# Performance work log

Measured on AMD Instinct MI355X. Metric: run time of the kernel, lower is better.

The kernel has to match this reference:

```python
import jax, jax.numpy as jnp
import numpy as np

N = 10000      # atoms
E = 100000     # edges
C = 64         # hidden channels
S = 16         # spherical harmonic components (l_max=3)
NB = 8         # Bessel basis size
HID = 64       # radial MLP hidden
NE = 10        # chemical elements
G = 64         # graphs in batch
L = 2          # interaction layers
HEADS = 1
RC = 5.0       # radial cutoff
AVG_NEI = 16.0


def _sph_l3(u):
    # real spherical harmonics up to l=3, component normalization, on unit vectors u [E,3]
    x, y, z = u[..., 0], u[..., 1], u[..., 2]
    s3 = 3.0 ** 0.5; s5 = 5.0 ** 0.5; s15 = 15.0 ** 0.5
    c1 = (35.0 / 8.0) ** 0.5; c2 = 105.0 ** 0.5; c3 = (21.0 / 8.0) ** 0.5
    c4 = (7.0 / 4.0) ** 0.5; c5 = (105.0 / 4.0) ** 0.5
    comps = [jnp.ones_like(x),
             s3 * x, s3 * y, s3 * z,
             s15 * x * y, s15 * y * z, (s5 / 2) * (3 * z * z - 1), s15 * x * z, (s15 / 2) * (x * x - y * y),
             c1 * y * (3 * x * x - y * y), c2 * x * y * z, c3 * y * (5 * z * z - 1), c4 * z * (5 * z * z - 3),
             c3 * x * (5 * z * z - 1), c5 * z * (x * x - y * y), c1 * x * (x * x - 3 * y * y)]
    return jnp.stack(comps, axis=-1)  # [E, 16]


def _radial(r):
    # Bessel radial basis * polynomial cutoff (p=6); r [E,1] -> [E, NB]
    n = jnp.arange(1, NB + 1, dtype=r.dtype)
    bessel = (2.0 / RC) ** 0.5 * jnp.sin(n * jnp.pi * r / RC) / r
    t = r / RC
    p = 6.0
    fcut = 1.0 - (p + 1) * (p + 2) / 2 * t ** p + p * (p + 2) * t ** (p + 1) - p * (p + 1) / 2 * t ** (p + 2)
    fcut = jnp.where(r < RC, fcut, 0.0)
    return bessel * fcut


def setup_inputs() -> dict:
    key = jax.random.key(0)
    ks = jax.random.split(key, 20)
    positions = jax.random.uniform(ks[0], (N, 3), dtype=jnp.float32) * 6.0
    species = jax.random.randint(ks[1], (N,), 0, NE)
    node_attrs = jax.nn.one_hot(species, NE, dtype=jnp.float32)
    sender = jax.random.randint(ks[2], (E,), 0, N)
    offs = jax.random.randint(ks[3], (E,), 1, N)
    receiver = (sender + offs) % N  # no self loops
    edge_index = jnp.stack([sender, receiver]).astype(jnp.int32)
    batch = jnp.sort(jax.random.randint(ks[4], (N,), 0, G)).astype(jnp.int32)
    head = jnp.zeros((G,), jnp.int32)
    shifts = jnp.zeros((E, 3), jnp.float32)
    ptr = jnp.arange(G + 1, dtype=jnp.int32)
    w = 0.1
    return {
        'positions': positions, 'node_attrs': node_attrs, 'shifts': shifts,
        'atomic_energies': jax.random.normal(ks[5], (HEADS, NE), jnp.float32),
        'W_emb': w * jax.random.normal(ks[6], (NE, C), jnp.float32),
        'W_up': w * jax.random.normal(ks[7], (L, C, C), jnp.float32),
        'mlp_w1': w * jax.random.normal(ks[8], (L, NB, HID), jnp.float32),
        'mlp_w2': w * jax.random.normal(ks[9], (L, HID, HID), jnp.float32),
        'mlp_w3': w * jax.random.normal(ks[10], (L, HID, C * S), jnp.float32),
        'W_mix': w * jax.random.normal(ks[11], (L, C, C), jnp.float32),
        'W_skip': w * jax.random.normal(ks[12], (L, C, NE, C), jnp.float32),
        'Wc': w * jax.random.normal(ks[13], (L, NE, 3, C), jnp.float32),
        'W_out': w * jax.random.normal(ks[14], (L, C, C), jnp.float32),
        'W_ro': w * jax.random.normal(ks[15], (L, C, HEADS), jnp.float32),
        'edge_index': edge_index, 'batch': batch, 'head': head, 'ptr': ptr,
    }


def reference(positions, node_attrs, shifts, atomic_energies, W_emb, W_up, mlp_w1,
              mlp_w2, mlp_w3, W_mix, W_skip, Wc, W_out, W_ro,
              edge_index, batch, head, ptr):
    n_nodes = positions.shape[0]
    n_graphs = ptr.shape[0] - 1
    sender, receiver = edge_index[0], edge_index[1]
    na = jnp.arange(n_nodes)
    node_heads = head[batch]                                   # [N]
    # isolated-atom reference energies
    node_e0 = (node_attrs @ atomic_energies.T)[na, node_heads]  # [N]
    e0 = jax.ops.segment_sum(node_e0, batch, num_segments=n_graphs)
    node_feats = node_attrs @ W_emb                            # [N, C]
    # edge geometry: gather positions by edge index
    vectors = positions[receiver] - positions[sender] + shifts  # [E, 3]
    lengths = jnp.sqrt(jnp.sum(vectors ** 2, axis=-1, keepdims=True))  # [E, 1]
    edge_attrs = _sph_l3(vectors / lengths)                    # [E, S]
    edge_feats = _radial(lengths)                              # [E, NB]
    energies = [e0, jnp.zeros_like(e0)]  # e0, pair_energy (no pair_repulsion)
    for l in range(W_up.shape[0]):
        # radial MLP -> per-edge tensor-product weights
        h = jax.nn.silu(edge_feats @ mlp_w1[l])
        h = jax.nn.silu(h @ mlp_w2[l])
        tp_w = (h @ mlp_w3[l]).reshape(-1, C, S)               # [E, C, S]
        up = node_feats @ W_up[l]                              # [N, C]
        # gather-compute-scatter message passing
        msg = up[sender][:, :, None] * edge_attrs[:, None, :] * tp_w  # [E, C, S]
        A = jax.ops.segment_sum(msg, receiver, num_segments=n_nodes) / AVG_NEI
        A = jnp.einsum('ncs,cd->nds', A, W_mix[l])             # [N, C, S]
        # element-conditioned skip connection
        sc = jnp.einsum('nc,ced,ne->nd', node_feats, W_skip[l], node_attrs)
        # symmetric-contraction product basis (correlation up to 3), element-conditioned
        w = jnp.einsum('ne,ekc->nkc', node_attrs, Wc[l])       # [N, 3, C]
        p1 = A[:, :, 0]
        p2 = jnp.einsum('ncs,ncs->nc', A, A)
        p3 = p2 * p1
        node_feats = (w[:, 0] * p1 + w[:, 1] * p2 + w[:, 2] * p3) @ W_out[l] + sc
        node_en = (node_feats @ W_ro[l])[na, node_heads]       # [N]
        energies.append(jax.ops.segment_sum(node_en, batch, num_segments=n_graphs))
    contributions = jnp.stack(energies, axis=-1)               # [G, L+2]
    return jnp.sum(contributions, axis=-1)                     # [G]
```

## Files before the change

### kernel.cpp

```cpp
#include <hip/hip_runtime.h>

typedef unsigned short u16;
typedef unsigned int u32;
typedef __attribute__((ext_vector_type(8))) short short8;
typedef __attribute__((ext_vector_type(4))) float f32x4;

#define N_NODES 10000
#define N_EDGES 100000
#define C_CH 64
#define S_SPH 16
#define NB_R 8
#define HID_D 64
#define NE_EL 10
#define G_GR 64
#define L_LAY 2
#define N_HEADS 1
#define RCUT 5.0f
#define INV_AVG (1.0f/16.0f)

__device__ __forceinline__ u16 f2bf(float f) {
  u32 u = __float_as_uint(f);
  u32 r = (u + 0x7FFFu + ((u >> 16) & 1u)) >> 16;
  return (u16)r;
}

__global__ void k_init0(float* __restrict__ out, int* __restrict__ deg) {
  int i = blockIdx.x * 256 + threadIdx.x;
  if (i < G_GR) out[i] = 0.0f;
  if (i < N_NODES) deg[i] = 0;
}

__global__ void k_node_init(const float* __restrict__ attrs, const float* __restrict__ ae,
                            const int* __restrict__ batch, const int* __restrict__ head,
                            int* __restrict__ species, float* __restrict__ out) {
  int n = blockIdx.x * 256 + threadIdx.x;
  if (n >= N_NODES) return;
  int sp = 0;
#pragma unroll
  for (int e = 0; e < NE_EL; ++e)
    if (attrs[n * NE_EL + e] > 0.5f) sp = e;
  species[n] = sp;
  int b = batch[n];
  int h = head[b];
  atomicAdd(&out[b], ae[h * NE_EL + sp]);
}

__global__ void k_embed(const int* __restrict__ species, const float* __restrict__ Wemb,
                        float* __restrict__ feats) {
  int idx = blockIdx.x * 256 + threadIdx.x;
  if (idx >= N_NODES * C_CH) return;
  feats[idx] = Wemb[species[idx >> 6] * C_CH + (idx & 63)];
}

__global__ void k_hist(const int* __restrict__ ei, int* __restrict__ deg) {
  int e = blockIdx.x * 256 + threadIdx.x;
  if (e >= N_EDGES) return;
  atomicAdd(&deg[ei[N_EDGES + e]], 1);
}

__global__ void __launch_bounds__(1024) k_scan(const int* __restrict__ deg,
                                               int* __restrict__ rowptr,
                                               int* __restrict__ woff) {
  __shared__ int wsum[16];
  __shared__ int carry_s;
  int tid = threadIdx.x;
  int lane = tid & 63, w = tid >> 6;
  if (tid == 0) carry_s = 0;
  __syncthreads();
  for (int base = 0; base < N_NODES; base += 1024) {
    int i = base + tid;
    int v = (i < N_NODES) ? deg[i] : 0;
    int orig = v;
#pragma unroll
    for (int off = 1; off < 64; off <<= 1) {
      int n = __shfl_up(v, off, 64);
      if (lane >= off) v += n;
    }
    if (lane == 63) wsum[w] = v;
    __syncthreads();
    if (w == 0 && lane < 16) {
      int x = wsum[lane];
#pragma unroll
      for (int off = 1; off < 16; off <<= 1) {
        int n = __shfl_up(x, off, 16);
        if (lane >= off) x += n;
      }
      wsum[lane] = x;
    }
    __syncthreads();
    int waveoff = (w > 0) ? wsum[w - 1] : 0;
    int carry = carry_s;
    int excl = carry + waveoff + v - orig;
    if (i < N_NODES) {
      rowptr[i] = excl;
      woff[i] = excl;
    }
    int tot = wsum[15];
    __syncthreads();
    if (tid == 0) carry_s = carry + tot;
    __syncthreads();
  }
  if (tid == 0) rowptr[N_NODES] = carry_s;
}

__global__ void k_permute(const int* __restrict__ ei, int* __restrict__ woff,
                          int* __restrict__ rank, int* __restrict__ sndp) {
  int e = blockIdx.x * 256 + threadIdx.x;
  if (e >= N_EDGES) return;
  int rdst = ei[N_EDGES + e];
  int pos = atomicAdd(&woff[rdst], 1);
  rank[e] = pos;
  sndp[pos] = ei[e];
}

__global__ void k_geom(const float* __restrict__ pos, const float* __restrict__ shifts,
                       const int* __restrict__ ei, const int* __restrict__ rank,
                       float* __restrict__ Yp, float* __restrict__ radp) {
  int e = blockIdx.x * 256 + threadIdx.x;
  if (e >= N_EDGES) return;
  int s = ei[e], r = ei[N_EDGES + e];
  float dx = pos[r * 3 + 0] - pos[s * 3 + 0] + shifts[e * 3 + 0];
  float dy = pos[r * 3 + 1] - pos[s * 3 + 1] + shifts[e * 3 + 1];
  float dz = pos[r * 3 + 2] - pos[s * 3 + 2] + shifts[e * 3 + 2];
  float rr = sqrtf(dx * dx + dy * dy + dz * dz);
  rr = fmaxf(rr, 1e-12f);
  float inv = 1.0f / rr;
  float x = dx * inv, y = dy * inv, z = dz * inv;
  float xx = x * x, yy = y * y, zz = z * z;
  const float s3 = 1.73205080757f, s5 = 2.2360679775f, s15 = 3.87298334621f;
  const float c1 = 2.09165006634f, c2 = 10.2469507659f, c3 = 1.62018517461f;
  const float c4 = 1.32287565553f, c5 = 5.12347538298f;
  int rk = rank[e];
  float4* Yo = (float4*)(Yp + (size_t)rk * 16);
  Yo[0] = make_float4(1.0f, s3 * x, s3 * y, s3 * z);
  Yo[1] = make_float4(s15 * x * y, s15 * y * z, 0.5f * s5 * (3.0f * zz - 1.0f), s15 * x * z);
  Yo[2] = make_float4(0.5f * s15 * (xx - yy), c1 * y * (3.0f * xx - yy), c2 * x * y * z,
                      c3 * y * (5.0f * zz - 1.0f));
  Yo[3] = make_float4(c4 * z * (5.0f * zz - 3.0f), c3 * x * (5.0f * zz - 1.0f),
                      c5 * z * (xx - yy), c1 * x * (xx - 3.0f * yy));
  float t = rr * (1.0f / RCUT);
  float t2 = t * t;
  float t6 = t2 * t2 * t2;
  float fcut = 1.0f - 28.0f * t6 + 48.0f * t6 * t - 21.0f * t6 * t2;
  if (rr >= RCUT) fcut = 0.0f;
  float pref = 0.63245553203f * inv * fcut;
  float arg = 3.14159265359f * rr * (1.0f / RCUT);
  float sa, ca;
  __sincosf(arg, &sa, &ca);
  float twoc = 2.0f * ca;
  float sprev = 0.0f, scur = sa;
  float rv[8];
#pragma unroll
  for (int n = 0; n < 8; ++n) {
    rv[n] = pref * scur;
    float snext = twoc * scur - sprev;
    sprev = scur;
    scur = snext;
  }
  float4* Ro = (float4*)(radp + (size_t)rk * 8);
  Ro[0] = make_float4(rv[0], rv[1], rv[2], rv[3]);
  Ro[1] = make_float4(rv[4], rv[5], rv[6], rv[7]);
}

__global__ void k_prep(const float* __restrict__ w3, const float* __restrict__ w2,
                       const float* __restrict__ wmix, const float* __restrict__ wskip,
                       u16* __restrict__ w3t, u16* __restrict__ w2t, u16* __restrict__ wmixf,
                       float* __restrict__ wskt) {
  int idx = blockIdx.x * 256 + threadIdx.x;
  if (idx < L_LAY * 65536) {
    int l = idx >> 16;
    int r = idx & 65535;
    int k = r & 63;
    int c = (r >> 6) & 63;
    int s = r >> 12;
    w3t[idx] = f2bf(w3[(l * 64 + k) * 1024 + c * 16 + s]);
  } else if (idx < L_LAY * 65536 + L_LAY * 4096) {
    int i = idx - L_LAY * 65536;
    int l = i >> 12;
    int r = i & 4095;
    int t = r >> 6;
    int j = r & 63;
    w2t[l * 4096 + t * 64 + j] = f2bf(w2[(l * 64 + j) * 64 + t]);
  } else if (idx < L_LAY * 65536 + 2 * L_LAY * 4096) {
    int i = idx - L_LAY * 65536 - L_LAY * 4096;
    int l = i >> 12;
    int r = i & 4095;
    int j = r & 7;
    int col = (r >> 3) & 15;
    int kg = (r >> 7) & 3;
    int hf = (r >> 9) & 1;
    int dc = (r >> 10) & 3;
    int c = hf * 32 + kg * 8 + j;
    int d = dc * 16 + col;
    wmixf[l * 4096 + r] = f2bf(wmix[(l * 64 + c) * 64 + d]);
  } else if (idx < L_LAY * 65536 + 2 * L_LAY * 4096 + L_LAY * 40960) {
    int i = idx - (L_LAY * 65536 + 2 * L_LAY * 4096);
    int l = (i >= 40960) ? 1 : 0;
    int r = i - l * 40960;
    int e = r >> 12;
    int rem = r & 4095;
    int c = rem >> 6;
    int d = rem & 63;
    wskt[(size_t)l * 40960 + e * 4096 + c * 64 + d] =
        wskip[(size_t)l * 40960 + c * 640 + e * 64 + d];
  }
}

__global__ void __launch_bounds__(64) k_edge_mlp(const float* __restrict__ radp,
                                                 const float* __restrict__ w1,
                                                 const u16* __restrict__ w2T,
                                                 u16* __restrict__ h2) {
  __shared__ float w1s[NB_R * HID_D];
  __shared__ __align__(16) u16 h1b[16 * 64];
  int lane = threadIdx.x;
  for (int i = lane; i < NB_R * HID_D; i += 64) w1s[i] = w1[i];
  int er = lane & 15, jg = lane >> 4;
  int eb = blockIdx.x * 16;
  int e = eb + er;
  float4 ra = *(const float4*)(radp + (size_t)e * 8);
  float4 rb = *(const float4*)(radp + (size_t)e * 8 + 4);
  float rv[8] = {ra.x, ra.y, ra.z, ra.w, rb.x, rb.y, rb.z, rb.w};
  u32* hb = (u32*)h1b;
#pragma unroll
  for (int jj = 0; jj < 16; jj += 2) {
    float p0 = 0.f, p1 = 0.f;
#pragma unroll
    for (int k = 0; k < 8; ++k) {
      p0 += rv[k] * w1s[k * 64 + jg * 16 + jj];
      p1 += rv[k] * w1s[k * 64 + jg * 16 + jj + 1];
    }
    p0 = p0 / (1.f + __expf(-p0));
    p1 = p1 / (1.f + __expf(-p1));
    u32 packed = (u32)f2bf(p0) | ((u32)f2bf(p1) << 16);
    int d = jg * 8 + (jj >> 1);
    hb[er * 32 + (d ^ ((er & 7) << 2))] = packed;
  }
  int row = er, kg = jg, col = er;
  const u32* hbr = (const u32*)h1b;
  short8 a0 = *(const short8*)&hbr[row * 32 + ((kg * 4) ^ ((row & 7) << 2))];
  short8 a1 = *(const short8*)&hbr[row * 32 + ((16 + kg * 4) ^ ((row & 7) << 2))];
#pragma unroll
  for (int ch = 0; ch < 4; ++ch) {
    const u16* wp = w2T + (ch * 16 + col) * 64 + kg * 8;
    short8 b0 = *(const short8*)wp;
    short8 b1 = *(const short8*)(wp + 32);
    f32x4 acc = {0.f, 0.f, 0.f, 0.f};
    acc = __builtin_amdgcn_mfma_f32_16x16x32_bf16(a0, b0, acc, 0, 0, 0);
    acc = __builtin_amdgcn_mfma_f32_16x16x32_bf16(a1, b1, acc, 0, 0, 0);
#pragma unroll
    for (int rr = 0; rr < 4; ++rr) {
      float v = acc[rr];
      v = v / (1.f + __expf(-v));
      h2[(size_t)(eb + kg * 4 + rr) * 64 + ch * 16 + col] = f2bf(v);
    }
  }
}

__global__ void __launch_bounds__(256) k_up(const float* __restrict__ feats,
                                            const float* __restrict__ Wup,
                                            float* __restrict__ up) {
  __shared__ float ws[C_CH * C_CH];
  __shared__ float fs[4][C_CH];
  int tid = threadIdx.x;
  for (int i = tid; i < C_CH * C_CH; i += 256) ws[i] = Wup[i];
  __syncthreads();
  int slot = tid >> 6, t = tid & 63;
  for (int nb = blockIdx.x * 4; nb < N_NODES; nb += gridDim.x * 4) {
    int n = nb + slot;
    fs[slot][t] = feats[n * C_CH + t];
    float acc = 0.0f;
#pragma unroll
    for (int j = 0; j < C_CH; ++j) acc += fs[slot][j] * ws[j * C_CH + t];
    up[n * C_CH + t] = acc * INV_AVG;
  }
}

__global__ void __launch_bounds__(256) k_upe(const float* __restrict__ up,
                                             const int* __restrict__ sndp,
                                             float* __restrict__ upe) {
  int tid = threadIdx.x;
  int slot = tid >> 6, t = tid & 63;
  for (int pb = blockIdx.x * 4; pb < N_EDGES; pb += gridDim.x * 4) {
    int pos = pb + slot;
    upe[(size_t)pos * 64 + t] = up[(size_t)sndp[pos] * 64 + t];
  }
}

__global__ void __launch_bounds__(256) k_gather_fused(
    const u16* __restrict__ h2, const u16* __restrict__ W3T, const float* __restrict__ upe,
    const float* __restrict__ Yp, const int* __restrict__ rowptr,
    const u16* __restrict__ WmixF, const float* __restrict__ featsOld,
    float* __restrict__ featsNew, const float* __restrict__ WskT,
    const float* __restrict__ Wc, const float* __restrict__ WoutG,
    const float* __restrict__ Wro, const int* __restrict__ species,
    const int* __restrict__ batch, const int* __restrict__ headArr,
    float* __restrict__ out) {
  __shared__ __align__(16) u16 h2s[128 * 64];
  __shared__ __align__(16) float Yts[16][128];
  __shared__ __align__(16) u16 Asub[4][16][72];
  __shared__ float qs[4][64];
  __shared__ float fsub[4][64];
  __shared__ int rps[5];
  int tid = threadIdx.x;
  int wv = tid >> 6, lane = tid & 63;
  int row = lane & 15, kg = lane >> 4;
  int col = row;
  int cg = wv;
  int cgc = cg * 16 + col;
  int nb = blockIdx.x * 4;
  if (tid < 5) rps[tid] = rowptr[nb + tid];
  fsub[wv][lane] = featsOld[(size_t)(nb + wv) * 64 + lane];
  __syncthreads();
  int rp0 = rps[0], rp1 = rps[1], rp2 = rps[2], rp3 = rps[3], rp4 = rps[4];
  int d0 = rp1 - rp0, d1 = rp2 - rp1, d2 = rp3 - rp2, d3 = rp4 - rp3;
  int rmax = max(max((d0 + 3) >> 2, (d1 + 3) >> 2), max((d2 + 3) >> 2, (d3 + 3) >> 2));
  rmax = max(rmax, 1);
  int baseR = kg == 0 ? rp0 : kg == 1 ? rp1 : kg == 2 ? rp2 : rp3;
  int degR = kg == 0 ? d0 : kg == 1 ? d1 : kg == 2 ? d2 : d3;

  float Areg[2][8];
#pragma unroll
  for (int hf = 0; hf < 2; ++hf)
#pragma unroll
    for (int ss = 0; ss < 8; ++ss) Areg[hf][ss] = 0.f;

  const u32* h2sr = (const u32*)h2s;

#pragma unroll 1
  for (int r0 = 0; r0 < rmax; r0 += 8) {
    int CH = min(8, rmax - r0);
    int shift = (CH > 4) ? 5 : 4;
    int nrows = 4 << shift;
    __syncthreads();
    for (int j = tid; j < nrows * 8; j += 256) {
      int rrow = j >> 3, part = j & 7;
      int node = rrow >> shift;
      int sl = r0 * 4 + (rrow & ((1 << shift) - 1));
      int e = min(rps[node] + sl, N_EDGES - 1);
      short8 v = *(const short8*)(h2 + (size_t)e * 64 + part * 8);
      int dsw = (part * 4) ^ (((rrow ^ (rrow >> 3)) & 7) << 2);
      *(short8*)((u32*)h2s + rrow * 32 + dsw) = v;
    }
    for (int j = tid; j < nrows * 4; j += 256) {
      int rrow = j >> 2, part = j & 3;
      int node = rrow >> shift;
      int sl = r0 * 4 + (rrow & ((1 << shift) - 1));
      int e = min(rps[node] + sl, N_EDGES - 1);
      float4 y = *(const float4*)(Yp + (size_t)e * 16 + part * 4);
      Yts[part * 4 + 0][rrow] = y.x;
      Yts[part * 4 + 1][rrow] = y.y;
      Yts[part * 4 + 2][rrow] = y.z;
      Yts[part * 4 + 3][rrow] = y.w;
    }
    __syncthreads();
#pragma unroll 1
    for (int hf = 0; hf < 2; ++hf) {
      short8 B0[8], B1[8];
#pragma unroll
      for (int ss = 0; ss < 8; ++ss) {
        int s = hf * 8 + ss;
        const u16* wp = W3T + (((s * 64 + cg * 16 + col) << 6) + kg * 8);
        B0[ss] = *(const short8*)wp;
        B1[ss] = *(const short8*)(wp + 32);
      }
#pragma unroll 1
      for (int rl = 0; rl < CH; ++rl) {
        int srow = ((row >> 2) << shift) + rl * 4 + (row & 3);
        int swz = (((srow ^ (srow >> 3)) & 7) << 2);
        short8 a0 = *(const short8*)(h2sr + srow * 32 + ((kg * 4) ^ swz));
        short8 a1 = *(const short8*)(h2sr + srow * 32 + ((16 + kg * 4) ^ swz));
        int slq = (r0 + rl) * 4;
        float upv[4];
#pragma unroll
        for (int q = 0; q < 4; ++q) {
          int pos = min(baseR + slq + q, N_EDGES - 1);
          float u = upe[(size_t)pos * 64 + cgc];
          upv[q] = (slq + q < degR) ? u : 0.f;
        }
        int ybase = (kg << shift) + rl * 4;
#pragma unroll
        for (int ss = 0; ss < 8; ++ss) {
          f32x4 acc = {0.f, 0.f, 0.f, 0.f};
          acc = __builtin_amdgcn_mfma_f32_16x16x32_bf16(a0, B0[ss], acc, 0, 0, 0);
          acc = __builtin_amdgcn_mfma_f32_16x16x32_bf16(a1, B1[ss], acc, 0, 0, 0);
          float4 yv = *(const float4*)&Yts[hf * 8 + ss][ybase];
          Areg[hf][ss] += acc[0] * yv.x * upv[0] + acc[1] * yv.y * upv[1] +
                          acc[2] * yv.z * upv[2] + acc[3] * yv.w * upv[3];
        }
      }
    }
  }
#pragma unroll
  for (int hf = 0; hf < 2; ++hf)
#pragma unroll
    for (int ss = 0; ss < 8; ++ss) Asub[kg][hf * 8 + ss][cg * 16 + col] = f2bf(Areg[hf][ss]);
  __syncthreads();

  int sp = species[nb + wv];
  short8 a0m = *(const short8*)&Asub[wv][row][kg * 8];
  short8 a1m = *(const short8*)&Asub[wv][row][32 + kg * 8];
#pragma unroll
  for (int dc = 0; dc < 4; ++dc) {
    short8 wf0 = *(const short8*)(WmixF + (size_t)(dc * 1024 + 0 * 512 + kg * 128 + row * 8));
    short8 wf1 = *(const short8*)(WmixF + (size_t)(dc * 1024 + 1 * 512 + kg * 128 + row * 8));
    f32x4 acc = {0.f, 0.f, 0.f, 0.f};
    acc = __builtin_amdgcn_mfma_f32_16x16x32_bf16(a0m, wf0, acc, 0, 0, 0);
    acc = __builtin_amdgcn_mfma_f32_16x16x32_bf16(a1m, wf1, acc, 0, 0, 0);
    float psq = acc[0] * acc[0] + acc[1] * acc[1] + acc[2] * acc[2] + acc[3] * acc[3];
    psq += __shfl_xor(psq, 16, 64);
    psq += __shfl_xor(psq, 32, 64);
    float p1 = __shfl(acc[0], lane & 15, 64);
    float p3 = psq * p1;
    int d = dc * 16 + row;
    float qv = Wc[(sp * 3 + 0) * 64 + d] * p1 + Wc[(sp * 3 + 1) * 64 + d] * psq +
               Wc[(sp * 3 + 2) * 64 + d] * p3;
    if (kg == 0) qs[wv][d] = qv;
  }

  int t = lane;
  const float* wsk = WskT + (size_t)sp * 4096;
  float sc = 0.f;
#pragma unroll 8
  for (int c = 0; c < 64; ++c) sc += fsub[wv][c] * wsk[c * 64 + t];
  float v = sc;
#pragma unroll 8
  for (int d = 0; d < 64; ++d) v += qs[wv][d] * WoutG[d * 64 + t];
  featsNew[(size_t)(nb + wv) * 64 + t] = v;
  int b = batch[nb + wv];
  float en = v * Wro[t * N_HEADS + headArr[b]];
#pragma unroll
  for (int off = 32; off; off >>= 1) en += __shfl_down(en, off, 64);
  if (lane == 0) atomicAdd(&out[b], en);
}

extern "C" void kernel_launch(void* const* d_in, const int* in_sizes, int n_in,
                              void* d_out, int out_size, void* d_ws, size_t ws_size,
                              hipStream_t stream) {
  const float* pos = (const float*)d_in[0];
  const float* attrs = (const float*)d_in[1];
  const float* shifts = (const float*)d_in[2];
  const float* ae = (const float*)d_in[3];
  const float* Wemb = (const float*)d_in[4];
  const float* Wup = (const float*)d_in[5];
  const float* w1 = (const float*)d_in[6];
  const float* w2 = (const float*)d_in[7];
  const float* w3 = (const float*)d_in[8];
  const float* Wmix = (const float*)d_in[9];
  const float* Wskip = (const float*)d_in[10];
  const float* Wc = (const float*)d_in[11];
  const float* Wout = (const float*)d_in[12];
  const float* Wro = (const float*)d_in[13];
  const int* ei = (const int*)d_in[14];
  const int* batch = (const int*)d_in[15];
  const int* head = (const int*)d_in[16];
  float* out = (float*)d_out;

  char* p = (char*)d_ws;
  float* Yp = (float*)p;     p += (size_t)N_EDGES * 16 * 4;
  float* radp = (float*)p;   p += (size_t)N_EDGES * 8 * 4;
  float* up = (float*)p;     p += (size_t)N_NODES * 64 * 4;
  float* upe = (float*)p;    p += (size_t)N_EDGES * 64 * 4;
  float* fA = (float*)p;     p += (size_t)N_NODES * 64 * 4;
  float* fB = (float*)p;     p += (size_t)N_NODES * 64 * 4;
  u16* h2 = (u16*)p;         p += (size_t)N_EDGES * 64 * 2;
  u16* W3T = (u16*)p;        p += (size_t)L_LAY * 65536 * 2;
  u16* w2T = (u16*)p;        p += (size_t)L_LAY * 4096 * 2;
  u16* WmixF = (u16*)p;      p += (size_t)L_LAY * 4096 * 2;
  float* WskT = (float*)p;   p += (size_t)L_LAY * 40960 * 4;
  int* species = (int*)p;    p += (size_t)N_NODES * 4;
  int* deg = (int*)p;        p += (size_t)N_NODES * 4;
  int* rowptr = (int*)p;     p += (size_t)(N_NODES + 4) * 4;
  int* woff = (int*)p;       p += (size_t)N_NODES * 4;
  int* rank = (int*)p;       p += (size_t)N_EDGES * 4;
  int* sndp = (int*)p;       p += (size_t)N_EDGES * 4;
  if ((size_t)(p - (char*)d_ws) > ws_size) return;

  k_init0<<<(N_NODES + 255) / 256, 256, 0, stream>>>(out, deg);
  k_node_init<<<(N_NODES + 255) / 256, 256, 0, stream>>>(attrs, ae, batch, head, species, out);
  k_embed<<<(N_NODES * C_CH + 255) / 256, 256, 0, stream>>>(species, Wemb, fA);
  k_hist<<<(N_EDGES + 255) / 256, 256, 0, stream>>>(ei, deg);
  k_scan<<<1, 1024, 0, stream>>>(deg, rowptr, woff);
  k_permute<<<(N_EDGES + 255) / 256, 256, 0, stream>>>(ei, woff, rank, sndp);
  k_geom<<<(N_EDGES + 255) / 256, 256, 0, stream>>>(pos, shifts, ei, rank, Yp, radp);
  int prepTot = L_LAY * 65536 + 2 * L_LAY * 4096 + L_LAY * 40960;
  k_prep<<<(prepTot + 255) / 256, 256, 0, stream>>>(w3, w2, Wmix, Wskip, W3T, w2T, WmixF, WskT);

  const float* fOld = fA;
  float* fNew = fB;
  for (int l = 0; l < L_LAY; ++l) {
    k_edge_mlp<<<N_EDGES / 16, 64, 0, stream>>>(radp, w1 + l * NB_R * HID_D, w2T + l * 4096, h2);
    k_up<<<512, 256, 0, stream>>>(fOld, Wup + l * C_CH * C_CH, up);
    k_upe<<<2048, 256, 0, stream>>>(up, sndp, upe);
    k_gather_fused<<<N_NODES / 4, 256, 0, stream>>>(
        h2, W3T + l * 65536, upe, Yp, rowptr, WmixF + l * 4096, fOld, fNew,
        WskT + (size_t)l * 40960, Wc + l * NE_EL * 3 * C_CH, Wout + l * C_CH * C_CH,
        Wro + l * C_CH * N_HEADS, species, batch, head, out);
    const float* tmp = fNew;
    fNew = (float*)fOld;
    fOld = tmp;
  }
}
```

Baseline: 452.0 us.

## Sort nodes by degree for balanced gather blocks and prefetch up values

Adds a counting sort of nodes by descending in-degree (bins, scan, scatter) so each gather block of four nodes processes nodes with similar degree, reducing padding wasted on the max-degree node. The gather kernel now uses fixed 4-row chunks with smaller shared tiles and prefetches the per-edge up values into registers before the staging barrier. This costs three extra small kernel launches and makes per-node reads and writes scattered instead of contiguous.

```diff
diff --git a/kernel.cpp b/kernel.cpp
--- a/kernel.cpp
+++ b/kernel.cpp
@@ -24,9 +24,10 @@
   return (u16)r;
 }
 
-__global__ void k_init0(float* __restrict__ out, int* __restrict__ deg) {
+__global__ void k_init0(float* __restrict__ out, int* __restrict__ deg, int* __restrict__ bins) {
   int i = blockIdx.x * 256 + threadIdx.x;
   if (i < G_GR) out[i] = 0.0f;
+  if (i < 64) bins[i] = 0;
   if (i < N_NODES) deg[i] = 0;
 }
 
@@ -101,6 +102,35 @@
     __syncthreads();
   }
   if (tid == 0) rowptr[N_NODES] = carry_s;
+}
+
+__global__ void k_degbin(const int* __restrict__ deg, int* __restrict__ bins) {
+  int n = blockIdx.x * 256 + threadIdx.x;
+  if (n >= N_NODES) return;
+  int d = min(deg[n], 63);
+  atomicAdd(&bins[63 - d], 1);
+}
+
+__global__ void __launch_bounds__(64) k_degscan(const int* __restrict__ bins,
+                                                int* __restrict__ binoff) {
+  int lane = threadIdx.x;
+  int v = bins[lane];
+  int orig = v;
+#pragma unroll
+  for (int off = 1; off < 64; off <<= 1) {
+    int t = __shfl_up(v, off, 64);
+    if (lane >= off) v += t;
+  }
+  binoff[lane] = v - orig;
+}
+
+__global__ void k_degscatter(const int* __restrict__ deg, int* __restrict__ binoff,
+                             int* __restrict__ nodeOrder) {
+  int n = blockIdx.x * 256 + threadIdx.x;
+  if (n >= N_NODES) return;
+  int d = min(deg[n], 63);
+  int pos = atomicAdd(&binoff[63 - d], 1);
+  nodeOrder[pos] = n;
 }
 
 __global__ void k_permute(const int* __restrict__ ei, int* __restrict__ woff,
@@ -289,18 +319,18 @@
 __global__ void __launch_bounds__(256) k_gather_fused(
     const u16* __restrict__ h2, const u16* __restrict__ W3T, const float* __restrict__ upe,
     const float* __restrict__ Yp, const int* __restrict__ rowptr,
-    const u16* __restrict__ WmixF, const float* __restrict__ featsOld,
-    float* __restrict__ featsNew, const float* __restrict__ WskT,
-    const float* __restrict__ Wc, const float* __restrict__ WoutG,
-    const float* __restrict__ Wro, const int* __restrict__ species,
-    const int* __restrict__ batch, const int* __restrict__ headArr,
-    float* __restrict__ out) {
-  __shared__ __align__(16) u16 h2s[128 * 64];
-  __shared__ __align__(16) float Yts[16][128];
+    const int* __restrict__ nodeOrder, const u16* __restrict__ WmixF,
+    const float* __restrict__ featsOld, float* __restrict__ featsNew,
+    const float* __restrict__ WskT, const float* __restrict__ Wc,
+    const float* __restrict__ WoutG, const float* __restrict__ Wro,
+    const int* __restrict__ species, const int* __restrict__ batch,
+    const int* __restrict__ headArr, float* __restrict__ out) {
+  __shared__ __align__(16) u16 h2s[64 * 64];
+  __shared__ __align__(16) float Yts[16][68];
   __shared__ __align__(16) u16 Asub[4][16][72];
   __shared__ float qs[4][64];
   __shared__ float fsub[4][64];
-  __shared__ int rps[5];
+  __shared__ int rpsA[4], rpsB[4];
   int tid = threadIdx.x;
   int wv = tid >> 6, lane = tid & 63;
   int row = lane & 15, kg = lane >> 4;
@@ -308,15 +338,19 @@
   int cg = wv;
   int cgc = cg * 16 + col;
   int nb = blockIdx.x * 4;
-  if (tid < 5) rps[tid] = rowptr[nb + tid];
-  fsub[wv][lane] = featsOld[(size_t)(nb + wv) * 64 + lane];
+  int nodeW = nodeOrder[nb + wv];
+  if (tid < 4) {
+    int n = nodeOrder[nb + tid];
+    rpsA[tid] = rowptr[n];
+    rpsB[tid] = rowptr[n + 1];
+  }
+  fsub[wv][lane] = featsOld[(size_t)nodeW * 64 + lane];
   __syncthreads();
-  int rp0 = rps[0], rp1 = rps[1], rp2 = rps[2], rp3 = rps[3], rp4 = rps[4];
-  int d0 = rp1 - rp0, d1 = rp2 - rp1, d2 = rp3 - rp2, d3 = rp4 - rp3;
-  int rmax = max(max((d0 + 3) >> 2, (d1 + 3) >> 2), max((d2 + 3) >> 2, (d3 + 3) >> 2));
-  rmax = max(rmax, 1);
-  int baseR = kg == 0 ? rp0 : kg == 1 ? rp1 : kg == 2 ? rp2 : rp3;
-  int degR = kg == 0 ? d0 : kg == 1 ? d1 : kg == 2 ? d2 : d3;
+  int dmax = 0;
+#pragma unroll
+  for (int i = 0; i < 4; ++i) dmax = max(dmax, rpsB[i] - rpsA[i]);
+  int rmax = max((dmax + 3) >> 2, 1);
+  int baseR = rpsA[kg], degR = rpsB[kg] - rpsA[kg];
 
   float Areg[2][8];
 #pragma unroll
@@ -327,25 +361,33 @@
   const u32* h2sr = (const u32*)h2s;
 
 #pragma unroll 1
-  for (int r0 = 0; r0 < rmax; r0 += 8) {
-    int CH = min(8, rmax - r0);
-    int shift = (CH > 4) ? 5 : 4;
-    int nrows = 4 << shift;
+  for (int r0 = 0; r0 < rmax; r0 += 4) {
+    int CH = min(4, rmax - r0);
+    float uval[16];
+#pragma unroll
+    for (int rl = 0; rl < 4; ++rl)
+#pragma unroll
+      for (int q = 0; q < 4; ++q) {
+        int slot = (r0 + rl) * 4 + q;
+        int pos = min(baseR + slot, N_EDGES - 1);
+        float u = upe[(size_t)pos * 64 + cgc];
+        uval[rl * 4 + q] = (slot < degR) ? u : 0.f;
+      }
     __syncthreads();
-    for (int j = tid; j < nrows * 8; j += 256) {
+    for (int j = tid; j < 512; j += 256) {
       int rrow = j >> 3, part = j & 7;
-      int node = rrow >> shift;
-      int sl = r0 * 4 + (rrow & ((1 << shift) - 1));
-      int e = min(rps[node] + sl, N_EDGES - 1);
+      int node = rrow >> 4;
+      int sl = r0 * 4 + (rrow & 15);
+      int e = min(rpsA[node] + sl, N_EDGES - 1);
       short8 v = *(const short8*)(h2 + (size_t)e * 64 + part * 8);
       int dsw = (part * 4) ^ (((rrow ^ (rrow >> 3)) & 7) << 2);
       *(short8*)((u32*)h2s + rrow * 32 + dsw) = v;
     }
-    for (int j = tid; j < nrows * 4; j += 256) {
-      int rrow = j >> 2, part = j & 3;
-      int node = rrow >> shift;
-      int sl = r0 * 4 + (rrow & ((1 << shift) - 1));
-      int e = min(rps[node] + sl, N_EDGES - 1);
+    {
+      int rrow = tid >> 2, part = tid & 3;
+      int node = rrow >> 4;
+      int sl = r0 * 4 + (rrow & 15);
+      int e = min(rpsA[node] + sl, N_EDGES - 1);
       float4 y = *(const float4*)(Yp + (size_t)e * 16 + part * 4);
       Yts[part * 4 + 0][rrow] = y.x;
       Yts[part * 4 + 1][rrow] = y.y;
@@ -365,27 +407,21 @@
       }
 #pragma unroll 1
       for (int rl = 0; rl < CH; ++rl) {
-        int srow = ((row >> 2) << shift) + rl * 4 + (row & 3);
+        int srow = (row >> 2) * 16 + rl * 4 + (row & 3);
         int swz = (((srow ^ (srow >> 3)) & 7) << 2);
         short8 a0 = *(const short8*)(h2sr + srow * 32 + ((kg * 4) ^ swz));
         short8 a1 = *(const short8*)(h2sr + srow * 32 + ((16 + kg * 4) ^ swz));
-        int slq = (r0 + rl) * 4;
-        float upv[4];
-#pragma unroll
-        for (int q = 0; q < 4; ++q) {
-          int pos = min(baseR + slq + q, N_EDGES - 1);
-          float u = upe[(size_t)pos * 64 + cgc];
-          upv[q] = (slq + q < degR) ? u : 0.f;
-        }
-        int ybase = (kg << shift) + rl * 4;
+        float u0 = uval[rl * 4 + 0], u1 = uval[rl * 4 + 1];
+        float u2 = uval[rl * 4 + 2], u3 = uval[rl * 4 + 3];
+        int ybase = kg * 16 + rl * 4;
 #pragma unroll
         for (int ss = 0; ss < 8; ++ss) {
           f32x4 acc = {0.f, 0.f, 0.f, 0.f};
           acc = __builtin_amdgcn_mfma_f32_16x16x32_bf16(a0, B0[ss], acc, 0, 0, 0);
           acc = __builtin_amdgcn_mfma_f32_16x16x32_bf16(a1, B1[ss], acc, 0, 0, 0);
           float4 yv = *(const float4*)&Yts[hf * 8 + ss][ybase];
-          Areg[hf][ss] += acc[0] * yv.x * upv[0] + acc[1] * yv.y * upv[1] +
-                          acc[2] * yv.z * upv[2] + acc[3] * yv.w * upv[3];
+          Areg[hf][ss] += acc[0] * yv.x * u0 + acc[1] * yv.y * u1 + acc[2] * yv.z * u2 +
+                          acc[3] * yv.w * u3;
         }
       }
     }
@@ -396,7 +432,7 @@
     for (int ss = 0; ss < 8; ++ss) Asub[kg][hf * 8 + ss][cg * 16 + col] = f2bf(Areg[hf][ss]);
   __syncthreads();
 
-  int sp = species[nb + wv];
+  int sp = species[nodeW];
   short8 a0m = *(const short8*)&Asub[wv][row][kg * 8];
   short8 a1m = *(const short8*)&Asub[wv][row][32 + kg * 8];
 #pragma unroll
@@ -425,8 +461,8 @@
   float v = sc;
 #pragma unroll 8
   for (int d = 0; d < 64; ++d) v += qs[wv][d] * WoutG[d * 64 + t];
-  featsNew[(size_t)(nb + wv) * 64 + t] = v;
-  int b = batch[nb + wv];
+  featsNew[(size_t)nodeW * 64 + t] = v;
+  int b = batch[nodeW];
   float en = v * Wro[t * N_HEADS + headArr[b]];
 #pragma unroll
   for (int off = 32; off; off >>= 1) en += __shfl_down(en, off, 64);
@@ -473,13 +509,19 @@
   int* woff = (int*)p;       p += (size_t)N_NODES * 4;
   int* rank = (int*)p;       p += (size_t)N_EDGES * 4;
   int* sndp = (int*)p;       p += (size_t)N_EDGES * 4;
+  int* bins = (int*)p;       p += 64 * 4;
+  int* binoff = (int*)p;     p += 64 * 4;
+  int* nodeOrder = (int*)p;  p += (size_t)N_NODES * 4;
   if ((size_t)(p - (char*)d_ws) > ws_size) return;
 
-  k_init0<<<(N_NODES + 255) / 256, 256, 0, stream>>>(out, deg);
+  k_init0<<<(N_NODES + 255) / 256, 256, 0, stream>>>(out, deg, bins);
   k_node_init<<<(N_NODES + 255) / 256, 256, 0, stream>>>(attrs, ae, batch, head, species, out);
   k_embed<<<(N_NODES * C_CH + 255) / 256, 256, 0, stream>>>(species, Wemb, fA);
   k_hist<<<(N_EDGES + 255) / 256, 256, 0, stream>>>(ei, deg);
   k_scan<<<1, 1024, 0, stream>>>(deg, rowptr, woff);
+  k_degbin<<<(N_NODES + 255) / 256, 256, 0, stream>>>(deg, bins);
+  k_degscan<<<1, 64, 0, stream>>>(bins, binoff);
+  k_degscatter<<<(N_NODES + 255) / 256, 256, 0, stream>>>(deg, binoff, nodeOrder);
   k_permute<<<(N_EDGES + 255) / 256, 256, 0, stream>>>(ei, woff, rank, sndp);
   k_geom<<<(N_EDGES + 255) / 256, 256, 0, stream>>>(pos, shifts, ei, rank, Yp, radp);
   int prepTot = L_LAY * 65536 + 2 * L_LAY * 4096 + L_LAY * 40960;
@@ -492,7 +534,7 @@
     k_up<<<512, 256, 0, stream>>>(fOld, Wup + l * C_CH * C_CH, up);
     k_upe<<<2048, 256, 0, stream>>>(up, sndp, upe);
     k_gather_fused<<<N_NODES / 4, 256, 0, stream>>>(
-        h2, W3T + l * 65536, upe, Yp, rowptr, WmixF + l * 4096, fOld, fNew,
+        h2, W3T + l * 65536, upe, Yp, rowptr, nodeOrder, WmixF + l * 4096, fOld, fNew,
         WskT + (size_t)l * 40960, Wc + l * NE_EL * 3 * C_CH, Wout + l * C_CH * C_CH,
         Wro + l * C_CH * N_HEADS, species, batch, head, out);
     const float* tmp = fNew;
```

New measurement: 459.1 us. Within noise of the previous version (+1.6%).
